# Optimization experiments

Hardware: AMD Instinct MI355X
Metric: run time of the kernel (lower is better)

The kernel has to match this reference:

```python
import jax, jax.numpy as jnp
import numpy as np

N = 100000  # nodes per cluster
E = 1000000  # nonzeros per sparse Laplacian
D = 64       # embedding_size
LEAKY_SLOPE = 0.2  # tf.nn.leaky_relu default alpha


def spmm(rows, cols, vals, dense, num_rows):
    """Sparse [num_rows, M] (COO) @ dense [M, D] -> [num_rows, D]."""
    gathered = vals[:, None] * dense[cols]  # [E, D]
    return jax.ops.segment_sum(gathered, rows, num_segments=num_rows)


def setup_inputs() -> dict:
    key = jax.random.key(0)
    ks = jax.random.split(key, 10)
    return {
        "ebs": jax.random.normal(ks[0], (N, D), dtype=jnp.float32),
        "entity_ebs": jax.random.normal(ks[1], (N, D), dtype=jnp.float32),
        "W_side": jax.random.normal(ks[2], (D, D), dtype=jnp.float32),
        "W_dot": jax.random.normal(ks[3], (D, D), dtype=jnp.float32),
        "LI_vals": jax.random.uniform(ks[4], (E,), dtype=jnp.float32),
        "L_vals": jax.random.uniform(ks[5], (E,), dtype=jnp.float32),
        "LI_rows": jax.random.randint(ks[6], (E,), 0, N, dtype=jnp.int32),
        "LI_cols": jax.random.randint(ks[7], (E,), 0, N, dtype=jnp.int32),
        "L_rows": jax.random.randint(ks[8], (E,), 0, N, dtype=jnp.int32),
        "L_cols": jax.random.randint(ks[9], (E,), 0, N, dtype=jnp.int32),
    }


def reference(ebs, entity_ebs, W_side, W_dot, LI_vals, L_vals,
              LI_rows, LI_cols, L_rows, L_cols) -> jnp.ndarray:
    # __build_weight_graph
    LI_side_embed = spmm(LI_rows, LI_cols, LI_vals, ebs, N)   # [N, D]
    L_side_embed = spmm(L_rows, L_cols, L_vals, ebs, N)       # [N, D]
    sum_embed = LI_side_embed @ W_side                          # [N, D]
    dot_embed = (L_side_embed * entity_ebs) @ W_dot             # [N, D]
    return jax.nn.leaky_relu(sum_embed + dot_embed, negative_slope=LEAKY_SLOPE)
```

## Files before the change

kernel.cpp:

```cpp
#include <hip/hip_runtime.h>

#define D        64
#define BINROWS  64
#define SUBCAP   256
#define NSHARD   8
#define NBINS_MAX 1568
#define CHUNK    4096
#define PER_TH   (CHUNK / 256)
#define FSTRIDE  68
#define SSEGCAP  2048
#define CURSTRIDE 16

typedef __attribute__((ext_vector_type(8))) short short8;
typedef __attribute__((ext_vector_type(4))) float floatx4;

__device__ __forceinline__ unsigned short f2bf(float f) {
    unsigned u = __float_as_uint(f);
    u += 0x7fffu + ((u >> 16) & 1u);
    return (unsigned short)(u >> 16);
}
__device__ __forceinline__ float bf2f(unsigned short u) {
    return __uint_as_float(((unsigned)u) << 16);
}

__global__ __launch_bounds__(256) void convert_kernel(
    const float* __restrict__ ebs, unsigned short* __restrict__ ebs16, int total4)
{
    int i = blockIdx.x * 256 + threadIdx.x;
    if (i >= total4) return;
    float4 v = ((const float4*)ebs)[i];
    ushort4 o;
    o.x = f2bf(v.x); o.y = f2bf(v.y); o.z = f2bf(v.z); o.w = f2bf(v.w);
    ((ushort4*)ebs16)[i] = o;
}

__global__ __launch_bounds__(256) void wfrag_kernel(
    const float* __restrict__ W_side, const float* __restrict__ W_dot,
    unsigned short* __restrict__ Wfrag)
{
    int t = blockIdx.x * 256 + threadIdx.x;
    int f = t >> 6;
    int l = t & 63;
    int jt = f >> 2, kt = f & 3;
    int q = l >> 4, nl = l & 15;
    int n = jt * 16 + nl;
#pragma unroll
    for (int j = 0; j < 8; ++j) {
        int k = kt * 32 + q * 8 + j;
        float w = (k < 64) ? W_side[k * 64 + n] : W_dot[(k - 64) * 64 + n];
        Wfrag[(size_t)f * 512 + l * 8 + j] = f2bf(w);
    }
}

__global__ __launch_bounds__(256) void expand_bin_kernel(
    const int* __restrict__ LI_rows, const int* __restrict__ LI_cols, const float* __restrict__ LI_vals,
    const int* __restrict__ L_rows,  const int* __restrict__ L_cols,  const float* __restrict__ L_vals,
    int* __restrict__ cursorP, uint2* __restrict__ seg, int E, int nbins)
{
    __shared__ uint2 sorted[CHUNK];
    __shared__ unsigned short sbin[CHUNK];
    __shared__ int hist[NBINS_MAX];
    __shared__ int offs[NBINS_MAX];
    __shared__ int cur[NBINS_MAX];
    __shared__ int gbase[NBINS_MAX];
    __shared__ int tsum[256];

    int t  = threadIdx.x;
    int c0 = blockIdx.x * CHUNK;
    int sh = blockIdx.x & (NSHARD - 1);
    int twoE = 2 * E;
    int chunkcnt = twoE - c0; if (chunkcnt > CHUNK) chunkcnt = CHUNK;

    for (int b = t; b < NBINS_MAX; b += 256) hist[b] = 0;
    __syncthreads();

    unsigned rm[PER_TH];
    uint2    cv[PER_TH];

#pragma unroll
    for (int k = 0; k < PER_TH; ++k) {
        int e = c0 + k * 256 + t;
        rm[k] = 0xFFFFFFFFu;
        if (e < twoE) {
            int m = (e >= E) ? 1 : 0;
            int r, cl; float v;
            if (m) { r = L_rows[e - E]; cl = L_cols[e - E]; v = L_vals[e - E]; }
            else   { r = LI_rows[e];    cl = LI_cols[e];    v = LI_vals[e]; }
            rm[k] = (unsigned)r | ((unsigned)m << 17);
            cv[k] = make_uint2((unsigned)cl, __float_as_uint(v));
            atomicAdd(&hist[r >> 6], 1);
        }
    }
    __syncthreads();

    int loc[7]; int tot = 0;
    if (t < 224) {
#pragma unroll
        for (int i = 0; i < 7; ++i) { loc[i] = tot; tot += hist[t * 7 + i]; }
    }
    tsum[t] = (t < 224) ? tot : 0;
    __syncthreads();
    for (int step = 1; step < 256; step <<= 1) {
        int add = (t >= step) ? tsum[t - step] : 0;
        __syncthreads();
        tsum[t] += add;
        __syncthreads();
    }
    int tbase = tsum[t] - ((t < 224) ? tot : 0);
    if (t < 224) {
#pragma unroll
        for (int i = 0; i < 7; ++i) {
            int key = t * 7 + i;
            int o = tbase + loc[i];
            offs[key] = o;
            cur[key]  = o;
        }
    }
    __syncthreads();

    for (int b = t; b < nbins; b += 256) {
        int c = hist[b];
        gbase[b] = c ? atomicAdd(&cursorP[(sh * NBINS_MAX + b) * CURSTRIDE], c) : 0;
    }

#pragma unroll
    for (int k = 0; k < PER_TH; ++k) {
        unsigned g = rm[k];
        if (g == 0xFFFFFFFFu) continue;
        int r   = (int)(g & 0x1FFFFu);
        int m   = (int)((g >> 17) & 1u);
        int bin = r >> 6;
        int rank = atomicAdd(&cur[bin], 1);
        sorted[rank] = make_uint2(((unsigned)m << 23) | ((unsigned)(r & 63) << 17) | cv[k].x, cv[k].y);
        sbin[rank]   = (unsigned short)bin;
    }
    __syncthreads();

    for (int i = t; i < chunkcnt; i += 256) {
        int bin = sbin[i];
        int pos = gbase[bin] + (i - offs[bin]);
        if (pos < SUBCAP)
            seg[((size_t)(sh * NBINS_MAX) + bin) * SUBCAP + pos] = sorted[i];
    }
}

__global__ __launch_bounds__(256) void fused_kernel(
    const uint2* __restrict__ seg, const int* __restrict__ cursorP,
    const unsigned short* __restrict__ ebs16,
    const float* __restrict__ entity,
    const unsigned short* __restrict__ Wfrag,
    float* __restrict__ out, int n)
{
    __shared__ __align__(16) char shmem[2 * BINROWS * FSTRIDE * 4];
    __shared__ int hist[128];
    __shared__ int offs[128];
    __shared__ int cur[128];
    uint2* sseg = (uint2*)shmem;
    float* facc = (float*)shmem;

    int t = threadIdx.x;
    int b = blockIdx.x;

    if (t < 128) hist[t] = 0;
    __syncthreads();

    int clen[NSHARD];
    uint2 held[NSHARD];
    unsigned hmask = 0;
#pragma unroll
    for (int sh = 0; sh < NSHARD; ++sh) {
        int c = cursorP[(sh * NBINS_MAX + b) * CURSTRIDE];
        clen[sh] = c < SUBCAP ? c : SUBCAP;
        if (t < clen[sh]) {
            held[sh] = seg[((size_t)(sh * NBINS_MAX) + b) * SUBCAP + t];
            hmask |= (1u << sh);
            atomicAdd(&hist[(held[sh].x >> 17) & 127u], 1);
        }
    }
    __syncthreads();

    if (t < 128) offs[t] = hist[t];
    __syncthreads();
    for (int step = 1; step < 128; step <<= 1) {
        int add = 0;
        if (t < 128 && t >= step) add = offs[t - step];
        __syncthreads();
        if (t < 128) offs[t] += add;
        __syncthreads();
    }
    if (t < 128) {
        int excl = offs[t] - hist[t];
        offs[t] = excl;
        cur[t]  = excl;
    }
    __syncthreads();

#pragma unroll
    for (int sh = 0; sh < NSHARD; ++sh) {
        if (hmask & (1u << sh)) {
            unsigned key = (held[sh].x >> 17) & 127u;
            int rank = atomicAdd(&cur[key], 1);
            sseg[rank] = held[sh];
        }
    }
    __syncthreads();

    int g  = t >> 4;
    int l4 = (t & 15) << 2;
    int beg[8], len[8], lenm1[8];
    int maxlen = 0;
#pragma unroll
    for (int kk = 0; kk < 8; ++kk) {
        int key = g * 8 + kk;
        beg[kk]   = offs[key];
        len[kk]   = hist[key];
        lenm1[kk] = len[kk] > 0 ? len[kk] - 1 : 0;
        maxlen = max(maxlen, len[kk]);
    }
    floatx4 a8[8];
#pragma unroll
    for (int kk = 0; kk < 8; ++kk) a8[kk] = (floatx4){0.f, 0.f, 0.f, 0.f};

    for (int s = 0; s < maxlen; ++s) {
#pragma unroll
        for (int kk = 0; kk < 8; ++kk) {
            bool sel = s < len[kk];
            int idx  = beg[kk] + min(s, lenm1[kk]);
            uint2 en = sseg[idx];
            unsigned enx = sel ? en.x : 0u;
            float vv = sel ? __uint_as_float(en.y) : 0.f;
            ushort4 x = *(const ushort4*)(ebs16 + (size_t)(enx & 0x1FFFFu) * D + l4);
            a8[kk][0] += vv * bf2f(x.x);
            a8[kk][1] += vv * bf2f(x.y);
            a8[kk][2] += vv * bf2f(x.z);
            a8[kk][3] += vv * bf2f(x.w);
        }
    }
    __syncthreads();

#pragma unroll
    for (int kk = 0; kk < 8; ++kk) {
        int key = g * 8 + kk;
        float* dst = facc + ((key >> 6) * BINROWS + (key & 63)) * FSTRIDE + l4;
        *(float4*)dst = make_float4(a8[kk][0], a8[kk][1], a8[kk][2], a8[kk][3]);
    }
    __syncthreads();

    int w = t >> 6;
    int l = t & 63;
    int q = l >> 4, mcol = l & 15;
    int rowbase = b * BINROWS + w * 16;
    int growA = rowbase + mcol;
    int binrow = w * 16 + mcol;
    const float* faccLI = facc;
    const float* faccL  = facc + BINROWS * FSTRIDE;

    floatx4 accv[4];
#pragma unroll
    for (int jt = 0; jt < 4; ++jt) accv[jt] = (floatx4){0.f, 0.f, 0.f, 0.f};

#pragma unroll
    for (int kt = 0; kt < 4; ++kt) {
        short8 af;
        if (kt < 2) {
            const float4* ap = (const float4*)(faccLI + binrow * FSTRIDE + kt * 32 + q * 8);
            float4 a0 = ap[0], a1 = ap[1];
            af[0] = (short)f2bf(a0.x); af[1] = (short)f2bf(a0.y);
            af[2] = (short)f2bf(a0.z); af[3] = (short)f2bf(a0.w);
            af[4] = (short)f2bf(a1.x); af[5] = (short)f2bf(a1.y);
            af[6] = (short)f2bf(a1.z); af[7] = (short)f2bf(a1.w);
        } else {
            const float4* lp = (const float4*)(faccL + binrow * FSTRIDE + (kt - 2) * 32 + q * 8);
            float4 l0 = lp[0], l1 = lp[1];
            float4 e0 = make_float4(0.f, 0.f, 0.f, 0.f), e1 = e0;
            if (growA < n) {
                const float4* ep = (const float4*)(entity + (size_t)growA * D + (kt - 2) * 32 + q * 8);
                e0 = ep[0]; e1 = ep[1];
            }
            af[0] = (short)f2bf(l0.x * e0.x); af[1] = (short)f2bf(l0.y * e0.y);
            af[2] = (short)f2bf(l0.z * e0.z); af[3] = (short)f2bf(l0.w * e0.w);
            af[4] = (short)f2bf(l1.x * e1.x); af[5] = (short)f2bf(l1.y * e1.y);
            af[6] = (short)f2bf(l1.z * e1.z); af[7] = (short)f2bf(l1.w * e1.w);
        }
#pragma unroll
        for (int jt = 0; jt < 4; ++jt) {
            const short8 bf = *(const short8*)(Wfrag + (size_t)(jt * 4 + kt) * 512 + (size_t)l * 8);
            accv[jt] = __builtin_amdgcn_mfma_f32_16x16x32_bf16(af, bf, accv[jt], 0, 0, 0);
        }
    }

#pragma unroll
    for (int jt = 0; jt < 4; ++jt) {
#pragma unroll
        for (int r = 0; r < 4; ++r) {
            int grow = rowbase + q * 4 + r;
            if (grow < n) {
                float v = accv[jt][r];
                v = v > 0.f ? v : 0.2f * v;
                out[(size_t)grow * D + jt * 16 + mcol] = v;
            }
        }
    }
}

__global__ void scatter_kernel(
    const float* __restrict__ LI_vals, const int* __restrict__ LI_rows, const int* __restrict__ LI_cols,
    const float* __restrict__ L_vals,  const int* __restrict__ L_rows,  const int* __restrict__ L_cols,
    const float* __restrict__ ebs,
    float* __restrict__ accLI, float* __restrict__ accL, int E)
{
    long long t = (long long)blockIdx.x * blockDim.x + threadIdx.x;
    long long e2 = t >> 4;
    if (e2 >= 2LL * E) return;
    int c = ((int)t & 15) << 2;
    const float* vals; const int* rows; const int* cols; float* acc; int e;
    if (e2 < E) { vals = LI_vals; rows = LI_rows; cols = LI_cols; acc = accLI; e = (int)e2; }
    else        { vals = L_vals;  rows = L_rows;  cols = L_cols;  acc = accL;  e = (int)(e2 - E); }
    float v = vals[e]; int r = rows[e]; int cl = cols[e];
    const float4 x = *(const float4*)(ebs + (size_t)cl * D + c);
    float* o = acc + (size_t)r * D + c;
    unsafeAtomicAdd(o + 0, v * x.x);
    unsafeAtomicAdd(o + 1, v * x.y);
    unsafeAtomicAdd(o + 2, v * x.z);
    unsafeAtomicAdd(o + 3, v * x.w);
}

__global__ __launch_bounds__(256) void epilogue_kernel(
    const float* __restrict__ acc, const float* __restrict__ entity,
    const float* __restrict__ W_side, const float* __restrict__ W_dot,
    float* __restrict__ out, int n)
{
    int lane = threadIdx.x & 63;
    int wave = (blockIdx.x << 2) | (threadIdx.x >> 6);
    int row  = (wave << 6) + lane;
    bool valid = row < n;
    const float* accLI = acc;
    const float* accL  = acc + (size_t)n * D;
    float a[D], b[D];
    if (valid) {
        const float4* ap = (const float4*)(accLI  + (size_t)row * D);
        const float4* lp = (const float4*)(accL   + (size_t)row * D);
        const float4* ep = (const float4*)(entity + (size_t)row * D);
#pragma unroll
        for (int qq = 0; qq < 16; ++qq) {
            float4 av = ap[qq]; float4 lv = lp[qq]; float4 ev = ep[qq];
            a[4*qq+0] = av.x; a[4*qq+1] = av.y; a[4*qq+2] = av.z; a[4*qq+3] = av.w;
            b[4*qq+0] = lv.x * ev.x; b[4*qq+1] = lv.y * ev.y;
            b[4*qq+2] = lv.z * ev.z; b[4*qq+3] = lv.w * ev.w;
        }
    } else {
#pragma unroll
        for (int qq = 0; qq < D; ++qq) { a[qq] = 0.f; b[qq] = 0.f; }
    }
    float4* op = (float4*)(out + (size_t)row * D);
#pragma unroll 1
    for (int jc = 0; jc < 16; ++jc) {
        float a0 = 0.f, a1 = 0.f, a2 = 0.f, a3 = 0.f;
#pragma unroll
        for (int k = 0; k < D; ++k) {
            float4 w1 = *(const float4*)(W_side + (k << 6) + (jc << 2));
            float4 w2 = *(const float4*)(W_dot  + (k << 6) + (jc << 2));
            a0 += a[k] * w1.x + b[k] * w2.x;
            a1 += a[k] * w1.y + b[k] * w2.y;
            a2 += a[k] * w1.z + b[k] * w2.z;
            a3 += a[k] * w1.w + b[k] * w2.w;
        }
        float4 r;
        r.x = a0 > 0.f ? a0 : 0.2f * a0;
        r.y = a1 > 0.f ? a1 : 0.2f * a1;
        r.z = a2 > 0.f ? a2 : 0.2f * a2;
        r.w = a3 > 0.f ? a3 : 0.2f * a3;
        if (valid) op[jc] = r;
    }
}

extern "C" void kernel_launch(void* const* d_in, const int* in_sizes, int n_in,
                              void* d_out, int out_size, void* d_ws, size_t ws_size,
                              hipStream_t stream) {
    const float* ebs     = (const float*)d_in[0];
    const float* entity  = (const float*)d_in[1];
    const float* W_side  = (const float*)d_in[2];
    const float* W_dot   = (const float*)d_in[3];
    const float* LI_vals = (const float*)d_in[4];
    const float* L_vals  = (const float*)d_in[5];
    const int*   LI_rows = (const int*)d_in[6];
    const int*   LI_cols = (const int*)d_in[7];
    const int*   L_rows  = (const int*)d_in[8];
    const int*   L_cols  = (const int*)d_in[9];
    float* out = (float*)d_out;

    int E = in_sizes[4];
    int n = in_sizes[0] / D;
    int nbins = (n + BINROWS - 1) / BINROWS;

    size_t curBytes = (size_t)NSHARD * NBINS_MAX * CURSTRIDE * sizeof(int);
    size_t segBytes = (size_t)NSHARD * NBINS_MAX * SUBCAP * sizeof(uint2);
    size_t ebsBytes = (size_t)n * D * sizeof(unsigned short);
    size_t wfBytes  = (size_t)16 * 512 * sizeof(unsigned short);
    size_t need = curBytes + segBytes + ebsBytes + wfBytes;

    if (ws_size >= need && nbins <= NBINS_MAX && n <= 131072) {
        int*            cursorP = (int*)d_ws;
        uint2*          seg     = (uint2*)((char*)d_ws + curBytes);
        unsigned short* ebs16   = (unsigned short*)((char*)d_ws + curBytes + segBytes);
        unsigned short* Wfrag   = (unsigned short*)((char*)d_ws + curBytes + segBytes + ebsBytes);

        hipMemsetAsync(cursorP, 0, curBytes, stream);

        int total4 = n * D / 4;
        convert_kernel<<<(total4 + 255) / 256, 256, 0, stream>>>(ebs, ebs16, total4);
        wfrag_kernel<<<4, 256, 0, stream>>>(W_side, W_dot, Wfrag);

        int xblocks = (2 * E + CHUNK - 1) / CHUNK;
        expand_bin_kernel<<<xblocks, 256, 0, stream>>>(
            LI_rows, LI_cols, LI_vals, L_rows, L_cols, L_vals,
            cursorP, seg, E, nbins);

        fused_kernel<<<nbins, 256, 0, stream>>>(
            seg, cursorP, ebs16, entity, Wfrag, out, n);
    } else {
        size_t accBytes = (size_t)2 * n * D * sizeof(float);
        float* acc   = (float*)d_ws;
        float* accLI = acc;
        float* accL  = accLI + (size_t)n * D;
        hipMemsetAsync(d_ws, 0, accBytes, stream);
        long long totalThreads = 2LL * E * 16;
        int sblocks = (int)((totalThreads + 255) / 256);
        scatter_kernel<<<sblocks, 256, 0, stream>>>(
            LI_vals, LI_rows, LI_cols, L_vals, L_rows, L_cols, ebs, accLI, accL, E);
        int nTiles = (n + 63) / 64;
        epilogue_kernel<<<(nTiles + 3) / 4, 256, 0, stream>>>(
            acc, entity, W_side, W_dot, out, n);
    }
}
```

Baseline: 231.0 us.

## Fold bf16 conversion and weight packing into binning kernel, store accumulators as bf16

The ebs bf16 conversion and W fragment packing now run inside expand_bin_kernel through a grid-stride loop, which removes two kernel launches. The bin chunk size shrinks from 4096 to 3072 and the offs array is dropped, lowering LDS use and raising block count. fused_kernel stores its per-row accumulators in LDS as bf16 rather than fp32, halving that buffer, and declares launch bounds for 8 blocks per CU. The extra bf16 rounding of the intermediate SpMM result adds a little precision loss.

```diff
diff --git a/kernel.cpp b/kernel.cpp
--- a/kernel.cpp
+++ b/kernel.cpp
@@ -5,10 +5,9 @@
 #define SUBCAP   256
 #define NSHARD   8
 #define NBINS_MAX 1568
-#define CHUNK    4096
+#define CHUNK    3072
 #define PER_TH   (CHUNK / 256)
-#define FSTRIDE  68
-#define SSEGCAP  2048
+#define FS16     72
 #define CURSTRIDE 16
 
 typedef __attribute__((ext_vector_type(8))) short short8;
@@ -23,49 +22,44 @@
     return __uint_as_float(((unsigned)u) << 16);
 }
 
-__global__ __launch_bounds__(256) void convert_kernel(
-    const float* __restrict__ ebs, unsigned short* __restrict__ ebs16, int total4)
-{
-    int i = blockIdx.x * 256 + threadIdx.x;
-    if (i >= total4) return;
-    float4 v = ((const float4*)ebs)[i];
-    ushort4 o;
-    o.x = f2bf(v.x); o.y = f2bf(v.y); o.z = f2bf(v.z); o.w = f2bf(v.w);
-    ((ushort4*)ebs16)[i] = o;
-}
-
-__global__ __launch_bounds__(256) void wfrag_kernel(
-    const float* __restrict__ W_side, const float* __restrict__ W_dot,
-    unsigned short* __restrict__ Wfrag)
-{
-    int t = blockIdx.x * 256 + threadIdx.x;
-    int f = t >> 6;
-    int l = t & 63;
-    int jt = f >> 2, kt = f & 3;
-    int q = l >> 4, nl = l & 15;
-    int n = jt * 16 + nl;
-#pragma unroll
-    for (int j = 0; j < 8; ++j) {
-        int k = kt * 32 + q * 8 + j;
-        float w = (k < 64) ? W_side[k * 64 + n] : W_dot[(k - 64) * 64 + n];
-        Wfrag[(size_t)f * 512 + l * 8 + j] = f2bf(w);
-    }
-}
-
 __global__ __launch_bounds__(256) void expand_bin_kernel(
     const int* __restrict__ LI_rows, const int* __restrict__ LI_cols, const float* __restrict__ LI_vals,
     const int* __restrict__ L_rows,  const int* __restrict__ L_cols,  const float* __restrict__ L_vals,
-    int* __restrict__ cursorP, uint2* __restrict__ seg, int E, int nbins)
+    int* __restrict__ cursorP, uint2* __restrict__ seg, int E, int nbins,
+    const float* __restrict__ ebs, unsigned short* __restrict__ ebs16, int total4,
+    const float* __restrict__ W_side, const float* __restrict__ W_dot,
+    unsigned short* __restrict__ Wfrag)
 {
     __shared__ uint2 sorted[CHUNK];
     __shared__ unsigned short sbin[CHUNK];
     __shared__ int hist[NBINS_MAX];
-    __shared__ int offs[NBINS_MAX];
     __shared__ int cur[NBINS_MAX];
     __shared__ int gbase[NBINS_MAX];
     __shared__ int tsum[256];
 
     int t  = threadIdx.x;
+
+    for (int i = blockIdx.x * 256 + t; i < total4; i += gridDim.x * 256) {
+        float4 v = ((const float4*)ebs)[i];
+        ushort4 o;
+        o.x = f2bf(v.x); o.y = f2bf(v.y); o.z = f2bf(v.z); o.w = f2bf(v.w);
+        ((ushort4*)ebs16)[i] = o;
+    }
+    if (blockIdx.x < 4) {
+        int tt = blockIdx.x * 256 + t;
+        int f = tt >> 6;
+        int l = tt & 63;
+        int jt = f >> 2, kt = f & 3;
+        int q = l >> 4, nl = l & 15;
+        int nn = jt * 16 + nl;
+#pragma unroll
+        for (int j = 0; j < 8; ++j) {
+            int k = kt * 32 + q * 8 + j;
+            float w = (k < 64) ? W_side[k * 64 + nn] : W_dot[(k - 64) * 64 + nn];
+            Wfrag[(size_t)f * 512 + l * 8 + j] = f2bf(w);
+        }
+    }
+
     int c0 = blockIdx.x * CHUNK;
     int sh = blockIdx.x & (NSHARD - 1);
     int twoE = 2 * E;
@@ -111,9 +105,7 @@
 #pragma unroll
         for (int i = 0; i < 7; ++i) {
             int key = t * 7 + i;
-            int o = tbase + loc[i];
-            offs[key] = o;
-            cur[key]  = o;
+            cur[key] = tbase + loc[i];
         }
     }
     __syncthreads();
@@ -138,25 +130,26 @@
 
     for (int i = t; i < chunkcnt; i += 256) {
         int bin = sbin[i];
-        int pos = gbase[bin] + (i - offs[bin]);
+        int off = cur[bin] - hist[bin];
+        int pos = gbase[bin] + (i - off);
         if (pos < SUBCAP)
             seg[((size_t)(sh * NBINS_MAX) + bin) * SUBCAP + pos] = sorted[i];
     }
 }
 
-__global__ __launch_bounds__(256) void fused_kernel(
+__global__ __launch_bounds__(256, 8) void fused_kernel(
     const uint2* __restrict__ seg, const int* __restrict__ cursorP,
     const unsigned short* __restrict__ ebs16,
     const float* __restrict__ entity,
     const unsigned short* __restrict__ Wfrag,
     float* __restrict__ out, int n)
 {
-    __shared__ __align__(16) char shmem[2 * BINROWS * FSTRIDE * 4];
+    __shared__ __align__(16) char shmem[2 * BINROWS * FS16 * 2];
     __shared__ int hist[128];
     __shared__ int offs[128];
     __shared__ int cur[128];
     uint2* sseg = (uint2*)shmem;
-    float* facc = (float*)shmem;
+    unsigned short* facc = (unsigned short*)shmem;
 
     int t = threadIdx.x;
     int b = blockIdx.x;
@@ -227,9 +220,8 @@
             bool sel = s < len[kk];
             int idx  = beg[kk] + min(s, lenm1[kk]);
             uint2 en = sseg[idx];
-            unsigned enx = sel ? en.x : 0u;
             float vv = sel ? __uint_as_float(en.y) : 0.f;
-            ushort4 x = *(const ushort4*)(ebs16 + (size_t)(enx & 0x1FFFFu) * D + l4);
+            ushort4 x = *(const ushort4*)(ebs16 + (size_t)(en.x & 0x1FFFFu) * D + l4);
             a8[kk][0] += vv * bf2f(x.x);
             a8[kk][1] += vv * bf2f(x.y);
             a8[kk][2] += vv * bf2f(x.z);
@@ -241,8 +233,10 @@
 #pragma unroll
     for (int kk = 0; kk < 8; ++kk) {
         int key = g * 8 + kk;
-        float* dst = facc + ((key >> 6) * BINROWS + (key & 63)) * FSTRIDE + l4;
-        *(float4*)dst = make_float4(a8[kk][0], a8[kk][1], a8[kk][2], a8[kk][3]);
+        ushort4 o;
+        o.x = f2bf(a8[kk][0]); o.y = f2bf(a8[kk][1]);
+        o.z = f2bf(a8[kk][2]); o.w = f2bf(a8[kk][3]);
+        *(ushort4*)(facc + ((size_t)(key >> 6) * BINROWS + (key & 63)) * FS16 + l4) = o;
     }
     __syncthreads();
 
@@ -252,8 +246,8 @@
     int rowbase = b * BINROWS + w * 16;
     int growA = rowbase + mcol;
     int binrow = w * 16 + mcol;
-    const float* faccLI = facc;
-    const float* faccL  = facc + BINROWS * FSTRIDE;
+    const unsigned short* faccLI = facc;
+    const unsigned short* faccL  = facc + BINROWS * FS16;
 
     floatx4 accv[4];
 #pragma unroll
@@ -263,24 +257,22 @@
     for (int kt = 0; kt < 4; ++kt) {
         short8 af;
         if (kt < 2) {
-            const float4* ap = (const float4*)(faccLI + binrow * FSTRIDE + kt * 32 + q * 8);
-            float4 a0 = ap[0], a1 = ap[1];
-            af[0] = (short)f2bf(a0.x); af[1] = (short)f2bf(a0.y);
-            af[2] = (short)f2bf(a0.z); af[3] = (short)f2bf(a0.w);
-            af[4] = (short)f2bf(a1.x); af[5] = (short)f2bf(a1.y);
-            af[6] = (short)f2bf(a1.z); af[7] = (short)f2bf(a1.w);
+            af = *(const short8*)(faccLI + (size_t)binrow * FS16 + kt * 32 + q * 8);
         } else {
-            const float4* lp = (const float4*)(faccL + binrow * FSTRIDE + (kt - 2) * 32 + q * 8);
-            float4 l0 = lp[0], l1 = lp[1];
+            short8 lv = *(const short8*)(faccL + (size_t)binrow * FS16 + (kt - 2) * 32 + q * 8);
             float4 e0 = make_float4(0.f, 0.f, 0.f, 0.f), e1 = e0;
             if (growA < n) {
                 const float4* ep = (const float4*)(entity + (size_t)growA * D + (kt - 2) * 32 + q * 8);
                 e0 = ep[0]; e1 = ep[1];
             }
-            af[0] = (short)f2bf(l0.x * e0.x); af[1] = (short)f2bf(l0.y * e0.y);
-            af[2] = (short)f2bf(l0.z * e0.z); af[3] = (short)f2bf(l0.w * e0.w);
-            af[4] = (short)f2bf(l1.x * e1.x); af[5] = (short)f2bf(l1.y * e1.y);
-            af[6] = (short)f2bf(l1.z * e1.z); af[7] = (short)f2bf(l1.w * e1.w);
+            af[0] = (short)f2bf(bf2f((unsigned short)lv[0]) * e0.x);
+            af[1] = (short)f2bf(bf2f((unsigned short)lv[1]) * e0.y);
+            af[2] = (short)f2bf(bf2f((unsigned short)lv[2]) * e0.z);
+            af[3] = (short)f2bf(bf2f((unsigned short)lv[3]) * e0.w);
+            af[4] = (short)f2bf(bf2f((unsigned short)lv[4]) * e1.x);
+            af[5] = (short)f2bf(bf2f((unsigned short)lv[5]) * e1.y);
+            af[6] = (short)f2bf(bf2f((unsigned short)lv[6]) * e1.z);
+            af[7] = (short)f2bf(bf2f((unsigned short)lv[7]) * e1.w);
         }
 #pragma unroll
         for (int jt = 0; jt < 4; ++jt) {
@@ -408,13 +400,11 @@
         hipMemsetAsync(cursorP, 0, curBytes, stream);
 
         int total4 = n * D / 4;
-        convert_kernel<<<(total4 + 255) / 256, 256, 0, stream>>>(ebs, ebs16, total4);
-        wfrag_kernel<<<4, 256, 0, stream>>>(W_side, W_dot, Wfrag);
-
         int xblocks = (2 * E + CHUNK - 1) / CHUNK;
         expand_bin_kernel<<<xblocks, 256, 0, stream>>>(
             LI_rows, LI_cols, LI_vals, L_rows, L_cols, L_vals,
-            cursorP, seg, E, nbins);
+            cursorP, seg, E, nbins,
+            ebs, ebs16, total4, W_side, W_dot, Wfrag);
 
         fused_kernel<<<nbins, 256, 0, stream>>>(
             seg, cursorP, ebs16, entity, Wfrag, out, n);
```

Measured after the change: 408.5 us. 76.8% more time.
